# Kernel tuning notes

Hardware: AMD Instinct MI355X
Metric: run time of the kernel (lower is better)

## Reference

```python
import jax, jax.numpy as jnp
import numpy as np

COMMITMENT_COST = 0.25


def setup_inputs() -> dict:
    key = jax.random.key(0)
    k1, k2 = jax.random.split(key)
    B, T, D = 32, 256, 512
    K = 8192
    x = jax.random.normal(k1, (B, T, D), dtype=jnp.float32)
    # nn.Embedding init: uniform(-1/K, 1/K)
    embeddings = jax.random.uniform(k2, (K, D), dtype=jnp.float32,
                                    minval=-1.0 / K, maxval=1.0 / K)
    return {"x": x, "embeddings": embeddings}


def reference(x, embeddings):
    orig_shape = x.shape
    D = orig_shape[-1]
    x_flat = x.reshape(-1, D)                      # [N, D]

    # squared Euclidean distances via expansion (argmin-equivalent to cdist)
    x_sq = jnp.sum(x_flat * x_flat, axis=1, keepdims=True)     # [N, 1]
    e_sq = jnp.sum(embeddings * embeddings, axis=1)            # [K]
    dots = jnp.einsum('nd,kd->nk', x_flat, embeddings)         # [N, K]
    distances = x_sq - 2.0 * dots + e_sq[None, :]              # [N, K]

    indices = jnp.argmin(distances, axis=1)                    # [N]
    quantized = embeddings[indices].reshape(orig_shape)        # [..., D]
    indices = indices.reshape(orig_shape[:-1])

    commitment_loss = jnp.mean((x - jax.lax.stop_gradient(quantized)) ** 2) * COMMITMENT_COST
    codebook_loss = jnp.mean((quantized - jax.lax.stop_gradient(x)) ** 2)
    total_loss = commitment_loss + codebook_loss

    # straight-through estimator
    quantized_st = x + jax.lax.stop_gradient(quantized - x)
    return quantized_st, indices, commitment_loss, codebook_loss, total_loss
```

## Files before the change

kernel.cpp:

```cpp
#include <hip/hip_runtime.h>

#define N_ROWS 8192
#define K_CODES 8192
#define D_DIM 512

typedef unsigned long long u64;

__global__ __launch_bounds__(256) void vq_sq(const float* __restrict__ x,
                                             const float* __restrict__ emb,
                                             float* __restrict__ x_sq,
                                             float* __restrict__ e_sq) {
  const int t = threadIdx.x;
  const int wave = t >> 6, l = t & 63;
  const int half = l >> 5, ll = l & 31;
  const int q = ll >> 3, j = ll & 7;
  const int row = blockIdx.x * 8 + wave * 2 + half;
  const float* p =
      (row < N_ROWS) ? (x + (size_t)row * D_DIM)
                     : (emb + (size_t)(row - N_ROWS) * D_DIM);
  const float v0 = p[128 * q + j];
  float r = __fmul_rn(v0, v0);
#pragma unroll
  for (int i = 1; i < 16; ++i) {
    const float v = p[128 * q + 8 * i + j];
    r = __fadd_rn(r, __fmul_rn(v, v));
  }
  r = __fadd_rn(r, __shfl_xor(r, 1, 64));
  r = __fadd_rn(r, __shfl_xor(r, 2, 64));
  r = __fadd_rn(r, __shfl_xor(r, 4, 64));
  r = __fadd_rn(r, __shfl_xor(r, 8, 64));
  r = __fadd_rn(r, __shfl_xor(r, 16, 64));
  if (ll == 0) {
    if (row < N_ROWS) x_sq[row] = r;
    else e_sq[row - N_ROWS] = r;
  }
}

__device__ __forceinline__ void compute_chunk(const float* __restrict__ esb,
                                              const float* __restrict__ xw,
                                              int dd0, int lane,
                                              float (&acc)[8][2]) {
  const int rbase = lane * 64;
  const int lm = lane & 7;
#pragma unroll
  for (int g = 0; g < 8; ++g) {
    const float* p = esb + rbase + 4 * (g ^ lm);
    const float4 ev0 = *reinterpret_cast<const float4*>(p);
    const float4 ev1 = *reinterpret_cast<const float4*>(p + 32);
#pragma unroll
    for (int r = 0; r < 8; ++r) {
      const float4 xv =
          *reinterpret_cast<const float4*>(xw + r * D_DIM + dd0 + 4 * g);
      float a0 = acc[r][0], a1 = acc[r][1];
      a0 = __fmaf_rn(xv.x, ev0.x, a0);
      a0 = __fmaf_rn(xv.y, ev0.y, a0);
      a0 = __fmaf_rn(xv.z, ev0.z, a0);
      a0 = __fmaf_rn(xv.w, ev0.w, a0);
      a1 = __fmaf_rn(xv.x, ev1.x, a1);
      a1 = __fmaf_rn(xv.y, ev1.y, a1);
      a1 = __fmaf_rn(xv.z, ev1.z, a1);
      a1 = __fmaf_rn(xv.w, ev1.w, a1);
      acc[r][0] = a0;
      acc[r][1] = a1;
    }
  }
}

#define STAGE1(BUF, DD0, I)                                                    \
  __builtin_amdgcn_global_load_lds(                                            \
      (const __attribute__((address_space(1))) void*)(                         \
          e + (size_t)(k0 + (t >> 3) + 64 * (I)) * D_DIM + (DD0) +             \
          4 * ((t & 7) ^ ((t >> 4) & 7))),                                     \
      (__attribute__((address_space(3))) void*)(&es[BUF][4 * t + 2048 * (I)]), \
      16, 0, 0)
#define STAGE(BUF, DD0)                                                        \
  do {                                                                         \
    STAGE1(BUF, DD0, 0);                                                       \
    STAGE1(BUF, DD0, 1);                                                       \
  } while (0)

__global__ __launch_bounds__(512, 2) void vq_dist(
    const float* __restrict__ x, const float* __restrict__ e,
    const float* __restrict__ x_sq, const float* __restrict__ e_sq,
    u64* __restrict__ slots) {
  __shared__ float es[2][4096];

  const int t = threadIdx.x;
  const int lane = t & 63;

  const int bx = blockIdx.x;
  const int swz = (bx & 7) * 1024 + (bx >> 3);
  const int kb = swz >> 7;
  const int nb = swz & 127;
  const int k0 = kb * 128;
  const int n0w = __builtin_amdgcn_readfirstlane(nb * 64 + (t >> 6) * 8);
  const float* xw = x + (size_t)n0w * D_DIM;

  float accA[8][2], accB[8][2];
#pragma unroll
  for (int r = 0; r < 8; ++r) {
    accA[r][0] = 0.0f; accA[r][1] = 0.0f;
    accB[r][0] = 0.0f; accB[r][1] = 0.0f;
  }

  STAGE(0, 0);
  asm volatile("s_waitcnt vmcnt(0)" ::: "memory");
  __syncthreads();

#pragma unroll 1
  for (int c = 0; c < 12; ++c) {
    STAGE((c + 1) & 1, (c + 1) * 32);
    compute_chunk(&es[c & 1][0], xw, c * 32, lane, accA);
    asm volatile("s_waitcnt vmcnt(0)" ::: "memory");
    __syncthreads();
  }
#pragma unroll 1
  for (int c = 12; c < 16; ++c) {
    if (c < 15) STAGE((c + 1) & 1, (c + 1) * 32);
    compute_chunk(&es[c & 1][0], xw, c * 32, lane, accB);
    asm volatile("s_waitcnt vmcnt(0)" ::: "memory");
    __syncthreads();
  }

  const float4 xsqa = *reinterpret_cast<const float4*>(x_sq + n0w);
  const float4 xsqb = *reinterpret_cast<const float4*>(x_sq + n0w + 4);
  const float xsq[8] = {xsqa.x, xsqa.y, xsqa.z, xsqa.w,
                        xsqb.x, xsqb.y, xsqb.z, xsqb.w};
  const int klane = k0 + 2 * lane;
  const float2 esq = *reinterpret_cast<const float2*>(e_sq + klane);
  const float esqv[2] = {esq.x, esq.y};

#pragma unroll
  for (int r = 0; r < 8; ++r) {
    u64 best = ~0ULL;
#pragma unroll
    for (int j = 0; j < 2; ++j) {
      float dot = __fadd_rn(accA[r][j], accB[r][j]);
      float dist = __fadd_rn(__fsub_rn(xsq[r], __fmul_rn(2.0f, dot)), esqv[j]);
      unsigned int b = __float_as_uint(dist);
      unsigned int sb = (b & 0x80000000u) ? ~b : (b | 0x80000000u);
      u64 key = ((u64)sb << 32) | (unsigned)(klane + j);
      best = best < key ? best : key;
    }
#pragma unroll
    for (int off = 32; off > 0; off >>= 1) {
      u64 o = __shfl_xor((unsigned long long)best, off, 64);
      best = best < o ? best : o;
    }
    if (lane == 0) atomicMin(&slots[n0w + r], best);
  }
}

__global__ __launch_bounds__(256) void vq_out(
    const float* __restrict__ x, const float* __restrict__ e,
    const u64* __restrict__ slots, float* __restrict__ out_q,
    float* __restrict__ out_idx, double* __restrict__ loss_part) {
  const int t = threadIdx.x;
  const int w = t >> 6, lane = t & 63;
  const int n = blockIdx.x * 4 + w;
  const int idx = (int)(slots[n] & 0xFFFFFFFFULL);
  const float4* qr = (const float4*)(e + (size_t)idx * D_DIM);
  const float4* xr = (const float4*)(x + (size_t)n * D_DIM);
  float4* outr = (float4*)(out_q + (size_t)n * D_DIM);
  double s = 0.0;
#pragma unroll
  for (int i = 0; i < 2; ++i) {
    const int d4 = lane * 2 + i;
    float4 q = qr[d4];
    float4 xv = xr[d4];
    outr[d4] = q;
    double d0 = (double)xv.x - (double)q.x;
    double d1 = (double)xv.y - (double)q.y;
    double d2 = (double)xv.z - (double)q.z;
    double d3 = (double)xv.w - (double)q.w;
    s += d0 * d0 + d1 * d1 + d2 * d2 + d3 * d3;
  }
  for (int off = 32; off > 0; off >>= 1) s += __shfl_down(s, off, 64);
  if (lane == 0) {
    out_idx[n] = (float)idx;
    atomicAdd(&loss_part[(n * 37) & 255], s);
  }
}

__global__ void vq_loss(const double* __restrict__ loss_part,
                        float* __restrict__ out_s) {
  __shared__ double sm[256];
  const int t = threadIdx.x;
  sm[t] = loss_part[t];
  __syncthreads();
  for (int off = 128; off > 0; off >>= 1) {
    if (t < off) sm[t] += sm[t + off];
    __syncthreads();
  }
  if (t == 0) {
    double m = sm[0] / (double)(N_ROWS * D_DIM);
    out_s[0] = (float)(0.25 * m);
    out_s[1] = (float)m;
    out_s[2] = (float)(1.25 * m);
  }
}

extern "C" void kernel_launch(void* const* d_in, const int* in_sizes, int n_in,
                              void* d_out, int out_size, void* d_ws, size_t ws_size,
                              hipStream_t stream) {
  const float* x = (const float*)d_in[0];
  const float* emb = (const float*)d_in[1];
  float* out = (float*)d_out;

  u64* slots = (u64*)d_ws;
  float* x_sq = (float*)((char*)d_ws + 65536);
  float* e_sq = (float*)((char*)d_ws + 98304);
  double* loss_part = (double*)((char*)d_ws + 131072);

  hipMemsetAsync(d_ws, 0xFF, 65536, stream);
  hipMemsetAsync(loss_part, 0, 256 * sizeof(double), stream);

  vq_sq<<<2048, 256, 0, stream>>>(x, emb, x_sq, e_sq);
  vq_dist<<<8192, 512, 0, stream>>>(x, emb, x_sq, e_sq, slots);
  vq_out<<<N_ROWS / 4, 256, 0, stream>>>(x, emb, slots, out,
                                         out + N_ROWS * D_DIM, loss_part);
  vq_loss<<<1, 256, 0, stream>>>(loss_part, out + N_ROWS * D_DIM + N_ROWS);
}
```

Baseline: 1.019 ms.

## Stage x tiles through LDS and remap blocks to XCDs in distance kernel

Each block now also stages its 64 x rows for the current 32-column chunk into double-buffered LDS with global_load_lds, so compute reads x from shared memory instead of issuing per-wave global/scalar loads. The block-to-tile mapping is changed so each XCD owns a contiguous range of row blocks, which improves L2 locality of x. Launch bounds raise the occupancy hint from 2 to 6 blocks per CU. The cost is extra LDS per block and higher register pressure under the tighter bound, with possible spills.

```diff
diff --git a/kernel.cpp b/kernel.cpp
--- a/kernel.cpp
+++ b/kernel.cpp
@@ -37,8 +37,8 @@
 }
 
 __device__ __forceinline__ void compute_chunk(const float* __restrict__ esb,
-                                              const float* __restrict__ xw,
-                                              int dd0, int lane,
+                                              const float* __restrict__ xsb,
+                                              int lane,
                                               float (&acc)[8][2]) {
   const int rbase = lane * 64;
   const int lm = lane & 7;
@@ -50,7 +50,7 @@
 #pragma unroll
     for (int r = 0; r < 8; ++r) {
       const float4 xv =
-          *reinterpret_cast<const float4*>(xw + r * D_DIM + dd0 + 4 * g);
+          *reinterpret_cast<const float4*>(xsb + r * 32 + 4 * g);
       float a0 = acc[r][0], a1 = acc[r][1];
       a0 = __fmaf_rn(xv.x, ev0.x, a0);
       a0 = __fmaf_rn(xv.y, ev0.y, a0);
@@ -66,35 +66,46 @@
   }
 }
 
-#define STAGE1(BUF, DD0, I)                                                    \
+#define STAGE_E(BUF, DD0, I)                                                   \
   __builtin_amdgcn_global_load_lds(                                            \
       (const __attribute__((address_space(1))) void*)(                         \
           e + (size_t)(k0 + (t >> 3) + 64 * (I)) * D_DIM + (DD0) +             \
           4 * ((t & 7) ^ ((t >> 4) & 7))),                                     \
       (__attribute__((address_space(3))) void*)(&es[BUF][4 * t + 2048 * (I)]), \
       16, 0, 0)
+#define STAGE_X(BUF, DD0)                                                      \
+  __builtin_amdgcn_global_load_lds(                                            \
+      (const __attribute__((address_space(1))) void*)(                         \
+          x + (size_t)(n0b + (t >> 3)) * D_DIM + (DD0) + 4 * (t & 7)),         \
+      (__attribute__((address_space(3))) void*)(&xs[BUF][4 * t]), 16, 0, 0)
 #define STAGE(BUF, DD0)                                                        \
   do {                                                                         \
-    STAGE1(BUF, DD0, 0);                                                       \
-    STAGE1(BUF, DD0, 1);                                                       \
+    STAGE_E(BUF, DD0, 0);                                                      \
+    STAGE_E(BUF, DD0, 1);                                                      \
+    STAGE_X(BUF, DD0);                                                         \
   } while (0)
 
-__global__ __launch_bounds__(512, 2) void vq_dist(
+__global__ __launch_bounds__(512, 6) void vq_dist(
     const float* __restrict__ x, const float* __restrict__ e,
     const float* __restrict__ x_sq, const float* __restrict__ e_sq,
     u64* __restrict__ slots) {
   __shared__ float es[2][4096];
+  __shared__ float xs[2][2048];
 
   const int t = threadIdx.x;
   const int lane = t & 63;
 
   const int bx = blockIdx.x;
-  const int swz = (bx & 7) * 1024 + (bx >> 3);
-  const int kb = swz >> 7;
-  const int nb = swz & 127;
+  const int xcd = bx & 7;
+  const int s = bx >> 3;
+  const int kb = s >> 4;
+  const int nb = xcd * 16 + (s & 15);
   const int k0 = kb * 128;
-  const int n0w = __builtin_amdgcn_readfirstlane(nb * 64 + (t >> 6) * 8);
-  const float* xw = x + (size_t)n0w * D_DIM;
+  const int n0b = nb * 64;
+  const int w = t >> 6;
+  const int n0w = __builtin_amdgcn_readfirstlane(n0b + w * 8);
+  const float* xsw_base0 = &xs[0][w * 256];
+  const float* xsw_base1 = &xs[1][w * 256];
 
   float accA[8][2], accB[8][2];
 #pragma unroll
@@ -110,14 +121,14 @@
 #pragma unroll 1
   for (int c = 0; c < 12; ++c) {
     STAGE((c + 1) & 1, (c + 1) * 32);
-    compute_chunk(&es[c & 1][0], xw, c * 32, lane, accA);
+    compute_chunk(&es[c & 1][0], (c & 1) ? xsw_base1 : xsw_base0, lane, accA);
     asm volatile("s_waitcnt vmcnt(0)" ::: "memory");
     __syncthreads();
   }
 #pragma unroll 1
   for (int c = 12; c < 16; ++c) {
     if (c < 15) STAGE((c + 1) & 1, (c + 1) * 32);
-    compute_chunk(&es[c & 1][0], xw, c * 32, lane, accB);
+    compute_chunk(&es[c & 1][0], (c & 1) ? xsw_base1 : xsw_base0, lane, accB);
     asm volatile("s_waitcnt vmcnt(0)" ::: "memory");
     __syncthreads();
   }
```

Result: slower. 2.923 ms (+186.8%).
